# Kernel tuning notes

Measured on AMD Instinct MI355X. Metric: run time of the kernel, lower is better.

Reference implementation:

```python
import math
import jax, jax.numpy as jnp
import numpy as np

# ---- module hyperparameters (from init_kwargs) ----
MAX_DISP = 48
IMG_WIDTH = 1248
W = IMG_WIDTH // 4          # 312 rows of the OT problem (left pixels)
C_COLS = MAX_DISP + W       # 360 columns (shifted right pixels)
NUM_ITER = 10
TAU = 0.95
EPS = 1.0
KAPPA = (1.0 - TAU) / 2.0
XI = (1.0 - TAU) / (1.0 + TAU)
RHO = EPS * TAU / (1.0 - TAU)
BIG_COST = 10000.0

B, H = 2, 64


def setup_inputs() -> dict:
    key = jax.random.key(0)
    scores = jax.random.normal(key, (B, MAX_DISP, H, W), dtype=jnp.float32)
    return {"scores": scores}


def _masked(x):
    # torch.where(isfinite(x), x, 0)
    return jnp.where(jnp.isfinite(x), x, jnp.zeros_like(x))


def _lse_kernel(Cm, f, g, axis):
    # S = (C - f[...,None] - g[...,None,:]) / eps ; eps*logsumexp(-S, axis)
    S = (Cm - f[..., None] - g[..., None, :]) / EPS
    w_res = EPS * jax.nn.logsumexp(-S, axis=axis)
    w_sgn = f if axis == -1 else g
    return w_res - _masked(w_sgn)


def _sinkhorn_update(Cm, f, g, axis, log_marginal):
    app = _lse_kernel(Cm, f, g, axis)
    return EPS * log_marginal - _masked(app)


def _smin(h, log_marginal):
    return -RHO * jax.nn.logsumexp(-h / RHO + log_marginal, axis=-1)


def _unbalanced_ot(Cm):
    # Cm: (B,H,W,C_COLS) cost matrix
    log_a = jnp.full((W,), -math.log(W), dtype=Cm.dtype)
    log_b = jnp.full((C_COLS,), -math.log(C_COLS), dtype=Cm.dtype)

    f = -EPS * jax.nn.logsumexp(-Cm / EPS + log_b, axis=-1)          # (B,H,W)
    g = jnp.zeros(Cm.shape[:2] + (C_COLS,), dtype=Cm.dtype)          # (B,H,C)

    for _ in range(NUM_ITER):
        old_f = f
        new_g = TAU * _sinkhorn_update(Cm, old_f, g, axis=-2, log_marginal=log_b)
        new_g = new_g - KAPPA * _smin(old_f, log_a)[..., None]
        new_g = new_g + XI * _smin(new_g, log_b)[..., None]
        new_f = TAU * _sinkhorn_update(Cm, f, new_g, axis=-1, log_marginal=log_a)
        new_f = new_f - KAPPA * _smin(new_g, log_b)[..., None]
        new_f = new_f + XI * _smin(new_f, log_a)[..., None]
        f, g = new_f, new_g

    S = (Cm - f[..., None] - g[..., None, :]) / EPS
    return jnp.exp(-S)                                               # transport plan P


def _scatter_to_cost(scores):
    # (B,D,H,W) scores -> (B,H,W,C_COLS) cost, vectorized scatter over d
    Bn, D, Hn, Wn = scores.shape
    j = jnp.arange(Wn)
    d = jnp.arange(D)
    col = j[None, :] - d[:, None] + MAX_DISP                          # (D,W), all in-range, no collisions
    jj = jnp.broadcast_to(j[None, :], (D, Wn))
    cost = jnp.full((Bn, Hn, Wn, C_COLS), BIG_COST, dtype=scores.dtype)
    # scores (B,D,H,W) -> (B,H,D,W) to match fancy-index result shape
    cost = cost.at[:, :, jj, col].set(-jnp.transpose(scores, (0, 2, 1, 3)))
    return cost


def _plan_to_disparity(P, D):
    right = jnp.arange(C_COLS, dtype=P.dtype) - D
    left = jnp.arange(W, dtype=P.dtype)
    disp_map = left[:, None] - right[None, :]                         # (W,C)
    mass = jnp.clip(jnp.sum(P, axis=-1), 1e-8, None)                  # (B,H,W)
    disp = jnp.sum(P * disp_map, axis=-1) / mass                      # (B,H,W)
    return disp[:, None, :, :]                                        # (B,1,H,W)


def reference(scores):
    D = scores.shape[1]
    Cm = _scatter_to_cost(scores)
    P = _unbalanced_ot(Cm)
    return _plan_to_disparity(P, D)
```

## Files before the change

kernel.cpp:

```cpp
#include <hip/hip_runtime.h>
#include <math.h>


#define MAXD   48
#define WROWS  312
#define CCOLS  360
#define NITER  10
#define NT     768
#define NWAVE  12
#define KD     24
#define NACC   (2 * NITER + 1)

__device__ __forceinline__ float pair_sum(float x) {
    int y = __builtin_amdgcn_update_dpp(0, __float_as_int(x), 0xB1, 0xf, 0xf, true);
    return x + __int_as_float(y);
}
template <int CTRL>
__device__ __forceinline__ float dpp_add(float x, float acc) {
    int y = __builtin_amdgcn_update_dpp(0, __float_as_int(x), CTRL, 0xf, 0xf, true);
    return acc + __int_as_float(y);
}
__device__ __forceinline__ float dpp_sum64(float x) {
    x = dpp_add<0x111>(x, x);
    x = dpp_add<0x112>(x, x);
    x = dpp_add<0x114>(x, x);
    x = dpp_add<0x118>(x, x);
    x = dpp_add<0x142>(x, x);
    x = dpp_add<0x143>(x, x);
    return x;
}

__global__ __launch_bounds__(NT)
void ot_disp_kernel(const float* __restrict__ scores, float* __restrict__ out) {
    const int bid  = blockIdx.x;
    const int tid  = threadIdx.x;
    const int half = tid >> 1;
    const int sub  = tid & 1;
    const int wid  = tid >> 6;

    const float LOG_A2 = -8.2854022f;
    const float LOG_B2 = -8.4918531f;
    const float TAU    = 0.95f;
    const float KAPPA  = 0.025f;
    const float XI     = 0.025641026f;
    const float RHO    = 19.0f;
    const float INVRHO = 0.052631579f;
    const float TIR    = 0.05f;

    __shared__ float2 sEA[204], sEB[205], sGA[180], sGB[181];
    __shared__ __align__(16) float s_red[NACC * NWAVE];
    __shared__ float s_R[NACC];
    float* const EAf = (float*)sEA;  float* const EBf = (float*)sEB;
    float* const GAf = (float*)sGA;  float* const GBf = (float*)sGB;

    if (tid < 205) {
        sEB[tid] = make_float2(0.f, 0.f);
        if (tid < 204) sEA[tid] = make_float2(0.f, 0.f);
        if (tid < 181) sGB[tid] = make_float2(0.f, 0.f);
        if (tid < 180) sGA[tid] = make_float2(0.f, 0.f);
    }

    const bool rowAct = (half < WROWS);
    const bool colAct = (half >= 1 && half < CCOLS);
    const int b = bid >> 6, h = bid & 63;
    const float* src = scores + ((size_t)(b * MAXD) * 64 + h) * WROWS;
    const size_t dstr = (size_t)64 * WROWS;
    const int d0 = sub * KD;
    const int jr = rowAct ? half : 0;
    const int jc = colAct ? half : 0;

    float wcol[KD];
    float wrowR[KD];
    #pragma unroll
    for (int m = 0; m < KD; ++m) {
        wrowR[m] = __expf(src[dstr * (size_t)(d0 + 23 - m) + jr]);
        int j = jc - MAXD + d0 + m;
        bool v = colAct && ((unsigned)j < (unsigned)WROWS);
        float sv = src[dstr * (size_t)(d0 + m) + (v ? j : 0)];
        wcol[m] = v ? __expf(sv) : 0.0f;
    }

    const int pe = jc + d0;
    const float2* const ep = (pe & 1) ? (sEB + ((pe + 1) >> 1)) : (sEA + (pe >> 1));
    const int qg = jr + 25 - d0;
    const float2* const gp = (qg & 1) ? (sGB + ((qg + 1) >> 1)) : (sGA + (qg >> 1));

    __syncthreads();

    {
        float a0=0,a1=0,a2=0,a3=0;
        #pragma unroll
        for (int m = 0; m < KD; m += 4) {
            a0 += wrowR[m];   a1 += wrowR[m+1];
            a2 += wrowR[m+2]; a3 += wrowR[m+3];
        }
        float s  = pair_sum((a0 + a1) + (a2 + a3));
        float ls = __builtin_amdgcn_logf(s);
        float eh = __builtin_amdgcn_exp2f(-ls);
        bool own = rowAct && (sub == 0);
        if (own) { EAf[half + MAXD] = eh; EBf[half + MAXD + 1] = eh; }
        float yv = __builtin_amdgcn_exp2f(fmaf(INVRHO, ls, LOG_A2));
        float t  = dpp_sum64(own ? yv : 0.0f);
        if ((tid & 63) == 63) s_red[0 * NWAVE + wid] = t;
        __syncthreads();
    }

    float2 gv[12];
    float ehat = 0.f, den = 0.f;
    for (int it = 0; it < NITER; ++it) {
        float a0=0,a1=0,a2=0,a3=0;
        #pragma unroll
        for (int u = 0; u < 12; u += 2) {
            float2 v0 = ep[u], v1 = ep[u+1];
            a0 = fmaf(wcol[2*u],   v0.x, a0);
            a1 = fmaf(wcol[2*u+1], v0.y, a1);
            a2 = fmaf(wcol[2*u+2], v1.x, a2);
            a3 = fmaf(wcol[2*u+3], v1.y, a3);
        }
        float cs  = pair_sum((a0 + a1) + (a2 + a3));
        float lcs = __builtin_amdgcn_logf(cs);
        float gh  = __builtin_amdgcn_exp2f(-TAU * lcs);
        bool ownC = colAct && (sub == 0);
        if (ownC) { GAf[half] = gh; GBf[half + 1] = gh; }
        float yv = __builtin_amdgcn_exp2f(fmaf(TIR, lcs, LOG_B2));
        float tg = dpp_sum64(ownC ? yv : 0.0f);
        if ((tid & 63) == 63) s_red[(1 + 2*it) * NWAVE + wid] = tg;
        __syncthreads();

        float b0=0,b1=0,b2=0,b3=0;
        #pragma unroll
        for (int u = 0; u < 12; u += 2) {
            gv[u] = gp[u]; gv[u+1] = gp[u+1];
            b0 = fmaf(wrowR[2*u],   gv[u].x,   b0);
            b1 = fmaf(wrowR[2*u+1], gv[u].y,   b1);
            b2 = fmaf(wrowR[2*u+2], gv[u+1].x, b2);
            b3 = fmaf(wrowR[2*u+3], gv[u+1].y, b3);
        }
        den = pair_sum((b0 + b1) + (b2 + b3));
        float lrs = __builtin_amdgcn_logf(den);
        ehat = __builtin_amdgcn_exp2f(-TAU * lrs);
        bool ownR = rowAct && (sub == 0);
        if (ownR) { EAf[half + MAXD] = ehat; EBf[half + MAXD + 1] = ehat; }
        float yf = __builtin_amdgcn_exp2f(fmaf(TIR, lrs, LOG_A2));
        float tf = dpp_sum64(ownR ? yf : 0.0f);
        if ((tid & 63) == 63) s_red[(2 + 2*it) * NWAVE + wid] = tf;
        __syncthreads();
    }

    if (tid < NACC) {
        const float4* rp = (const float4*)(s_red + tid * NWAVE);
        float4 a = rp[0], b = rp[1], c = rp[2];
        float s = ((a.x + a.y) + (a.z + a.w))
                + (((b.x + b.y) + (b.z + b.w)) + ((c.x + c.y) + (c.z + c.w)));
        s_R[tid] = __builtin_amdgcn_logf(s);
    }
    __syncthreads();

    float fsh   = -LOG_B2;
    float sminF = fsh - RHO * s_R[0];
    float gsh   = 0.f;
    #pragma unroll
    for (int it = 0; it < NITER; ++it) {
        float Cg = TAU * (LOG_B2 - fsh) - KAPPA * sminF;
        float sg = Cg - RHO * s_R[1 + 2*it];
        gsh = Cg + XI * sg;
        float sminG = (1.0f + XI) * sg;
        float Cf = TAU * (LOG_A2 - gsh) - KAPPA * sminG;
        float sf = Cf - RHO * s_R[2 + 2*it];
        fsh   = Cf + XI * sf;
        sminF = (1.0f + XI) * sf;
    }

    float n0 = 0.f, n1 = 0.f;
    #pragma unroll
    for (int u = 0; u < 12; ++u) {
        n0 = fmaf((float)(d0 + 23 - 2*u) * wrowR[2*u],   gv[u].x, n0);
        n1 = fmaf((float)(d0 + 22 - 2*u) * wrowR[2*u+1], gv[u].y, n1);
    }
    float num = pair_sum(n0 + n1);
    if (rowAct && sub == 0) {
        float E = __builtin_amdgcn_exp2f(fsh + gsh) * ehat;
        float mass = fmaxf(E * den, 1e-8f);
        out[(size_t)bid * WROWS + half] = (E * num) / mass;
    }
}

extern "C" void kernel_launch(void* const* d_in, const int* in_sizes, int n_in,
                              void* d_out, int out_size, void* d_ws, size_t ws_size,
                              hipStream_t stream) {
    const float* scores = (const float*)d_in[0];
    float* out = (float*)d_out;
    ot_disp_kernel<<<128, NT, 0, stream>>>(scores, out);
}
```

Before: 24.65 us.

## Defer per-iteration marginal reductions to a single post-loop pass over stored logs

```diff
diff --git a/kernel.cpp b/kernel.cpp
--- a/kernel.cpp
+++ b/kernel.cpp
@@ -30,7 +30,7 @@
     return x;
 }
 
-__global__ __launch_bounds__(NT)
+__global__ __launch_bounds__(NT, 3)
 void ot_disp_kernel(const float* __restrict__ scores, float* __restrict__ out) {
     const int bid  = blockIdx.x;
     const int tid  = threadIdx.x;
@@ -48,11 +48,19 @@
     const float TIR    = 0.05f;
 
     __shared__ float2 sEA[204], sEB[205], sGA[180], sGB[181];
-    __shared__ __align__(16) float s_red[NACC * NWAVE];
+    __shared__ __align__(16) float s_lg[NACC][384];
     __shared__ float s_R[NACC];
     float* const EAf = (float*)sEA;  float* const EBf = (float*)sEB;
     float* const GAf = (float*)sGA;  float* const GBf = (float*)sGB;
 
+    {
+        float4* lg4 = (float4*)&s_lg[0][0];
+        #pragma unroll
+        for (int i = 0; i < 3; ++i) {
+            int idx = tid + i * NT;
+            if (idx < NACC * 96) lg4[idx] = make_float4(-1e30f, -1e30f, -1e30f, -1e30f);
+        }
+    }
     if (tid < 205) {
         sEB[tid] = make_float2(0.f, 0.f);
         if (tid < 204) sEA[tid] = make_float2(0.f, 0.f);
@@ -97,11 +105,10 @@
         float s  = pair_sum((a0 + a1) + (a2 + a3));
         float ls = __builtin_amdgcn_logf(s);
         float eh = __builtin_amdgcn_exp2f(-ls);
-        bool own = rowAct && (sub == 0);
-        if (own) { EAf[half + MAXD] = eh; EBf[half + MAXD + 1] = eh; }
-        float yv = __builtin_amdgcn_exp2f(fmaf(INVRHO, ls, LOG_A2));
-        float t  = dpp_sum64(own ? yv : 0.0f);
-        if ((tid & 63) == 63) s_red[0 * NWAVE + wid] = t;
+        if (rowAct && sub == 0) {
+            EAf[half + MAXD] = eh; EBf[half + MAXD + 1] = eh;
+            s_lg[0][half] = ls;
+        }
         __syncthreads();
     }
 
@@ -120,11 +127,10 @@
         float cs  = pair_sum((a0 + a1) + (a2 + a3));
         float lcs = __builtin_amdgcn_logf(cs);
         float gh  = __builtin_amdgcn_exp2f(-TAU * lcs);
-        bool ownC = colAct && (sub == 0);
-        if (ownC) { GAf[half] = gh; GBf[half + 1] = gh; }
-        float yv = __builtin_amdgcn_exp2f(fmaf(TIR, lcs, LOG_B2));
-        float tg = dpp_sum64(ownC ? yv : 0.0f);
-        if ((tid & 63) == 63) s_red[(1 + 2*it) * NWAVE + wid] = tg;
+        if (colAct && sub == 0) {
+            GAf[half] = gh; GBf[half + 1] = gh;
+            s_lg[1 + 2*it][half] = lcs;
+        }
         __syncthreads();
 
         float b0=0,b1=0,b2=0,b3=0;
@@ -139,22 +145,27 @@
         den = pair_sum((b0 + b1) + (b2 + b3));
         float lrs = __builtin_amdgcn_logf(den);
         ehat = __builtin_amdgcn_exp2f(-TAU * lrs);
-        bool ownR = rowAct && (sub == 0);
-        if (ownR) { EAf[half + MAXD] = ehat; EBf[half + MAXD + 1] = ehat; }
-        float yf = __builtin_amdgcn_exp2f(fmaf(TIR, lrs, LOG_A2));
-        float tf = dpp_sum64(ownR ? yf : 0.0f);
-        if ((tid & 63) == 63) s_red[(2 + 2*it) * NWAVE + wid] = tf;
-        __syncthreads();
-    }
-
-    if (tid < NACC) {
-        const float4* rp = (const float4*)(s_red + tid * NWAVE);
-        float4 a = rp[0], b = rp[1], c = rp[2];
-        float s = ((a.x + a.y) + (a.z + a.w))
-                + (((b.x + b.y) + (b.z + b.w)) + ((c.x + c.y) + (c.z + c.w)));
-        s_R[tid] = __builtin_amdgcn_logf(s);
-    }
-    __syncthreads();
+        if (rowAct && sub == 0) {
+            EAf[half + MAXD] = ehat; EBf[half + MAXD + 1] = ehat;
+            s_lg[2 + 2*it][half] = lrs;
+        }
+        __syncthreads();
+    }
+
+    {
+        const int lane = tid & 63;
+        for (int t = wid; t < NACC; t += NWAVE) {
+            const float coef = (t == 0) ? INVRHO : TIR;
+            const float cst  = (t & 1)  ? LOG_B2 : LOG_A2;
+            float s = 0.f;
+            #pragma unroll
+            for (int k = 0; k < 6; ++k)
+                s += __builtin_amdgcn_exp2f(fmaf(coef, s_lg[t][lane + 64*k], cst));
+            s = dpp_sum64(s);
+            if (lane == 63) s_R[t] = __builtin_amdgcn_logf(s);
+        }
+        __syncthreads();
+    }
 
     float fsh   = -LOG_B2;
     float sminF = fsh - RHO * s_R[0];
```

Result: no change. 24.56 us (-0.4%).
